# Kernel tuning notes

Hardware: AMD Instinct MI355X
Metric: run time of the kernel (lower is better)

Reference implementation:

```python
import jax, jax.numpy as jnp
import numpy as np

EMBED_DIM = 1024
NUM_HEADS = 16
HEAD_DIM = EMBED_DIM // NUM_HEADS


def setup_inputs() -> dict:
    key = jax.random.key(0)
    ks = jax.random.split(key, 5)
    B, S, D = 2, 2048, EMBED_DIM
    scale_w = 1.0 / np.sqrt(D)
    x = jax.random.normal(ks[0], (B, S, D), dtype=jnp.float32)
    Wq = jax.random.normal(ks[1], (D, D), dtype=jnp.float32) * scale_w
    Wk = jax.random.normal(ks[2], (D, D), dtype=jnp.float32) * scale_w
    Wv = jax.random.normal(ks[3], (D, D), dtype=jnp.float32) * scale_w
    Wo = jax.random.normal(ks[4], (D, D), dtype=jnp.float32) * scale_w
    return {"x": x, "Wq": Wq, "Wk": Wk, "Wv": Wv, "Wo": Wo}


def reference(x, Wq, Wk, Wv, Wo):
    B, S, D = x.shape
    H, Dh = NUM_HEADS, HEAD_DIM
    scale = 1.0 / jnp.sqrt(jnp.asarray(Dh, dtype=x.dtype))

    def split_heads(t):
        return t.reshape(B, S, H, Dh).transpose(0, 2, 1, 3)  # [B,H,S,Dh]

    q = split_heads(x @ Wq)
    k = split_heads(x @ Wk)
    v = split_heads(x @ Wv)

    scores = jnp.einsum("bhqd,bhkd->bhqk", q, k) * scale
    causal = jnp.tril(jnp.ones((S, S), dtype=bool))[None, None]
    scores = jnp.where(causal, scores, jnp.asarray(-1e9, dtype=scores.dtype))
    weights = jax.nn.softmax(scores, axis=-1)
    attn = jnp.einsum("bhqk,bhkd->bhqd", weights, v)
    attn = attn.transpose(0, 2, 1, 3).reshape(B, S, D)
    return attn @ Wo
```

## Files before the change

### kernel.cpp

```cpp
#include <hip/hip_runtime.h>
#include <cstdint>

typedef __bf16 bf16;
typedef __bf16 bf16x2 __attribute__((ext_vector_type(2)));
typedef __bf16 bf16x4 __attribute__((ext_vector_type(4)));
typedef __bf16 bf16x8 __attribute__((ext_vector_type(8)));
typedef float f32x4 __attribute__((ext_vector_type(4)));

constexpr int S = 2048, D = 1024, H = 16, HD = 64, B = 2;
constexpr size_t TSZ = (size_t)B * H * S * HD;

__device__ __forceinline__ f32x4 mfma16(bf16x8 a, bf16x8 b, f32x4 c) {
  return __builtin_amdgcn_mfma_f32_16x16x32_bf16(a, b, c, 0, 0, 0);
}

__device__ __forceinline__ void gl_lds16(const bf16* g, bf16* s) {
  __builtin_amdgcn_global_load_lds((__attribute__((address_space(1))) void*)g,
                                   (__attribute__((address_space(3))) void*)s,
                                   16, 0, 0);
}

__global__ __launch_bounds__(256) void prep_all(const float* __restrict__ x,
                                                const float* __restrict__ W0,
                                                const float* __restrict__ W1,
                                                const float* __restrict__ W2,
                                                const float* __restrict__ W3,
                                                bf16* __restrict__ xb,
                                                bf16* __restrict__ Wt) {
  __shared__ __align__(16) bf16 Lt[64][68];
  const int bid = blockIdx.x, t = threadIdx.x;
  if (bid < 2048) {
    const size_t i = (size_t)bid * 256 + t;
    const float4 a = ((const float4*)x)[2 * i];
    const float4 b = ((const float4*)x)[2 * i + 1];
    bf16x8 o = {(bf16)a.x, (bf16)a.y, (bf16)a.z, (bf16)a.w,
                (bf16)b.x, (bf16)b.y, (bf16)b.z, (bf16)b.w};
    *(bf16x8*)&xb[i * 8] = o;
    return;
  }
  const int r = bid - 2048;
  const int z = r >> 8, rest = r & 255;
  const float* W = z == 0 ? W0 : z == 1 ? W1 : z == 2 ? W2 : W3;
  const int k0 = (rest & 15) * 64, n0 = (rest >> 4) * 64;
  const int tr = t >> 4, tc = (t & 15) * 4;
#pragma unroll
  for (int p = 0; p < 4; ++p) {
    const int rr = 16 * p + tr;
    const float4 v = *(const float4*)&W[(size_t)(k0 + rr) * D + n0 + tc];
    Lt[tc + 0][rr] = (bf16)v.x;
    Lt[tc + 1][rr] = (bf16)v.y;
    Lt[tc + 2][rr] = (bf16)v.z;
    Lt[tc + 3][rr] = (bf16)v.w;
  }
  __syncthreads();
#pragma unroll
  for (int p = 0; p < 4; ++p) {
    const int n = 16 * p + tr;
    const bf16x4 o = *(const bf16x4*)&Lt[n][tc];
    *(bf16x4*)&Wt[((size_t)z * D + n0 + n) * D + k0 + tc] = o;
  }
}

template <int MODE, int BNT>
__global__ __launch_bounds__(256) void gemm_bt(const bf16* __restrict__ A,
                                               const bf16* __restrict__ Bt,
                                               void* __restrict__ Cp) {
  constexpr int K = 1024;
  constexpr int NI = BNT / 32;
  __shared__ __align__(16) bf16 As[128 * 64];
  __shared__ __align__(16) bf16 Bs[BNT * 64];

  const int bid = blockIdx.x, nwg = gridDim.x;
  const int lg = (bid & 7) * (nwg >> 3) + (bid >> 3);
  const int bm = (lg & 31) * 128;
  const int bn = (lg >> 5) * BNT;

  const int t = threadIdx.x, l = t & 63, w = t >> 6;
  const int c = l & 15, g = l >> 4, cx = c & 7;
  const int lrow = l >> 3;
  const int srcc = ((l & 7) ^ lrow) << 3;
  const int wm = (w >> 1) * 64, wn = (w & 1) * (BNT / 2);

  f32x4 acc[4][NI] = {};

  for (int kt = 0; kt < K / 64; ++kt) {
    const int k0 = kt * 64;
    __syncthreads();
#pragma unroll
    for (int i = 0; i < 4; ++i) {
      const int ci = i * 4 + w;
      const int row = ci * 8 + lrow;
      gl_lds16(A + (size_t)(bm + row) * K + k0 + srcc, As + ci * 512 + l * 8);
    }
#pragma unroll
    for (int i = 0; i < BNT / 32; ++i) {
      const int ci = i * 4 + w;
      const int row = ci * 8 + lrow;
      gl_lds16(Bt + (size_t)(bn + row) * K + k0 + srcc, Bs + ci * 512 + l * 8);
    }
    __syncthreads();

    bf16x8 af[4][2], bfv[NI][2];
#pragma unroll
    for (int mi = 0; mi < 4; ++mi) {
      const int row = wm + mi * 16 + c;
#pragma unroll
      for (int kh = 0; kh < 2; ++kh)
        af[mi][kh] = *(const bf16x8*)&As[row * 64 + (((kh * 4 + g) ^ cx) << 3)];
    }
#pragma unroll
    for (int ni = 0; ni < NI; ++ni) {
      const int row = wn + ni * 16 + c;
#pragma unroll
      for (int kh = 0; kh < 2; ++kh)
        bfv[ni][kh] = *(const bf16x8*)&Bs[row * 64 + (((kh * 4 + g) ^ cx) << 3)];
    }
#pragma unroll
    for (int mi = 0; mi < 4; ++mi)
#pragma unroll
      for (int ni = 0; ni < NI; ++ni) {
        acc[mi][ni] = mfma16(af[mi][0], bfv[ni][0], acc[mi][ni]);
        acc[mi][ni] = mfma16(af[mi][1], bfv[ni][1], acc[mi][ni]);
      }
  }

#pragma unroll
  for (int mi = 0; mi < 4; ++mi)
#pragma unroll
    for (int ni = 0; ni < NI; ++ni)
#pragma unroll
      for (int r = 0; r < 4; ++r) {
        const int m = bm + wm + mi * 16 + 4 * g + r;
        const int n = bn + wn + ni * 16 + c;
        const float v = acc[mi][ni][r];
        if constexpr (MODE == 0) {
          const int which = n >> 10, nn = n & 1023;
          const int h = nn >> 6, d = nn & 63;
          const int bb = m >> 11, s = m & 2047;
          ((bf16*)Cp)[which * TSZ + ((((size_t)bb * H + h) * S + s) << 6) + d] =
              (bf16)v;
        } else {
          ((float*)Cp)[(size_t)m * D + n] = v;
        }
      }
}

__global__ __launch_bounds__(256, 4) void attn11(const bf16* __restrict__ Q,
                                                 const bf16* __restrict__ Kg,
                                                 const bf16* __restrict__ Vg,
                                                 bf16* __restrict__ O) {
  __shared__ __align__(16) bf16 Ks[64 * 64];
  __shared__ __align__(16) bf16 Vt[64 * 64];

  const int bid = blockIdx.x;
  const int bh = bid & 31, j = bid >> 5;
  const int t = threadIdx.x, l = t & 63, w = t >> 6;
  const int c = l & 15, g = l >> 4, cx = c & 7;
  const int bb = bh >> 4, h = bh & 15;
  const float SC = 0.18033688011112042f;
  const float THRS = 44.3614195558365f;

  const bf16* Kbase = Kg + (size_t)bh * S * HD;
  const bf16* Vbase = Vg + (size_t)bh * S * HD;

  const int kv0 = t >> 3, dg0 = t & 7;
  const int kv1 = kv0 + 32;
  const int p2 = t & 31, dgv = t >> 5;
  const int hv = p2 >> 4;
  const int gv = (p2 >> 1) & 3;
  const int jv = ((p2 >> 3) & 1) * 4 + (p2 & 1) * 2;
  const int vchunk = (hv << 2) | gv;

  for (int ph = 0; ph < 2; ++ph) {
    const int qt = ph ? (31 - j) : j;
    const int q0 = qt * 64;
    const int qglob = q0 + 16 * w + c;
    const bf16* Qrow = Q + ((size_t)bh * S + qglob) * HD;
    const bf16x8 qf0 = *(const bf16x8*)&Qrow[g * 8];
    const bf16x8 qf1 = *(const bf16x8*)&Qrow[32 + g * 8];

    bf16x8 ka0 = *(const bf16x8*)&Kbase[kv0 * 64 + dg0 * 8];
    bf16x8 ka1 = *(const bf16x8*)&Kbase[kv1 * 64 + dg0 * 8];
    bf16x8 va0 = *(const bf16x8*)&Vbase[(2 * p2) * 64 + dgv * 8];
    bf16x8 va1 = *(const bf16x8*)&Vbase[(2 * p2 + 1) * 64 + dgv * 8];

    f32x4 oacc[4] = {};
    float mrun = -1e30f, lrun = 0.f;

    for (int kt = 0; kt <= qt; ++kt) {
      __builtin_amdgcn_s_barrier();
      __builtin_amdgcn_sched_barrier(0);

      *(bf16x8*)&Ks[kv0 * 64 + ((dg0 ^ (kv0 & 7)) << 3)] = ka0;
      *(bf16x8*)&Ks[kv1 * 64 + ((dg0 ^ (kv1 & 7)) << 3)] = ka1;
#pragma unroll
      for (int i = 0; i < 8; ++i) {
        bf16x2 pr2 = {va0[i], va1[i]};
        *(bf16x2*)&Vt[(8 * dgv + i) * 64 + ((vchunk ^ i) << 3) + jv] = pr2;
      }
      bf16x8 kn0 = ka0, kn1 = ka1, vn0 = va0, vn1 = va1;
      if (kt < qt) {
        const bf16* Kt = Kbase + (size_t)(kt + 1) * 64 * HD;
        const bf16* Vs = Vbase + (size_t)(kt + 1) * 64 * HD;
        kn0 = *(const bf16x8*)&Kt[kv0 * 64 + dg0 * 8];
        kn1 = *(const bf16x8*)&Kt[kv1 * 64 + dg0 * 8];
        vn0 = *(const bf16x8*)&Vs[(2 * p2) * 64 + dgv * 8];
        vn1 = *(const bf16x8*)&Vs[(2 * p2 + 1) * 64 + dgv * 8];
      }
      asm volatile("s_waitcnt lgkmcnt(0)" ::: "memory");
      __builtin_amdgcn_s_barrier();
      __builtin_amdgcn_sched_barrier(0);

      f32x4 st[4];
      __builtin_amdgcn_s_setprio(1);
#pragma unroll
      for (int ct = 0; ct < 4; ++ct) {
        const int krow = ct * 16 + c;
        const bf16x8 kf0 = *(const bf16x8*)&Ks[krow * 64 + ((g ^ cx) << 3)];
        const bf16x8 kf1 = *(const bf16x8*)&Ks[krow * 64 + (((4 + g) ^ cx) << 3)];
        f32x4 z = {};
        z = mfma16(kf0, qf0, z);
        st[ct] = mfma16(kf1, qf1, z);
      }
      __builtin_amdgcn_s_setprio(0);

      if (kt == qt) {
#pragma unroll
        for (int ct = 0; ct < 4; ++ct)
#pragma unroll
          for (int r = 0; r < 4; ++r)
            if (kt * 64 + ct * 16 + 4 * g + r > qglob) st[ct][r] = -1e30f;
      }

      float tm[4];
#pragma unroll
      for (int ct = 0; ct < 4; ++ct)
        tm[ct] = fmaxf(fmaxf(st[ct][0], st[ct][1]), fmaxf(st[ct][2], st[ct][3]));
      float mt = fmaxf(fmaxf(tm[0], tm[1]), fmaxf(tm[2], tm[3]));
      mt = fmaxf(mt, __shfl_xor(mt, 16));
      mt = fmaxf(mt, __shfl_xor(mt, 32));
      if (!__all(mt <= mrun + THRS)) {
        const float mnew = fmaxf(mrun, mt);
        const float fac = __builtin_amdgcn_exp2f((mrun - mnew) * SC);
        lrun *= fac;
#pragma unroll
        for (int ct = 0; ct < 4; ++ct)
#pragma unroll
          for (int r = 0; r < 4; ++r) oacc[ct][r] *= fac;
        mrun = mnew;
      }
      float p[4][4];
      float sq[4];
#pragma unroll
      for (int ct = 0; ct < 4; ++ct) {
#pragma unroll
        for (int r = 0; r < 4; ++r)
          p[ct][r] = __builtin_amdgcn_exp2f((st[ct][r] - mrun) * SC);
        sq[ct] = (p[ct][0] + p[ct][1]) + (p[ct][2] + p[ct][3]);
      }
      lrun += (sq[0] + sq[1]) + (sq[2] + sq[3]);

      const bf16x8 pa0 = {(bf16)p[0][0], (bf16)p[0][1], (bf16)p[0][2], (bf16)p[0][3],
                          (bf16)p[1][0], (bf16)p[1][1], (bf16)p[1][2], (bf16)p[1][3]};
      const bf16x8 pa1 = {(bf16)p[2][0], (bf16)p[2][1], (bf16)p[2][2], (bf16)p[2][3],
                          (bf16)p[3][0], (bf16)p[3][1], (bf16)p[3][2], (bf16)p[3][3]};

      __builtin_amdgcn_s_setprio(1);
#pragma unroll
      for (int ct = 0; ct < 4; ++ct) {
        const int vrow = ct * 16 + c;
        const bf16x8 vt0 = *(const bf16x8*)&Vt[vrow * 64 + ((g ^ cx) << 3)];
        const bf16x8 vt1 = *(const bf16x8*)&Vt[vrow * 64 + (((4 + g) ^ cx) << 3)];
        oacc[ct] = mfma16(vt0, pa0, oacc[ct]);
        oacc[ct] = mfma16(vt1, pa1, oacc[ct]);
      }
      __builtin_amdgcn_s_setprio(0);

      ka0 = kn0; ka1 = kn1; va0 = vn0; va1 = vn1;
    }

    float lt = lrun;
    lt += __shfl_xor(lt, 16);
    lt += __shfl_xor(lt, 32);
    const float inv = 1.f / lt;
    bf16* Orow = O + ((size_t)bb * S + qglob) * D + h * 64;
#pragma unroll
    for (int ct = 0; ct < 4; ++ct)
#pragma unroll
      for (int pr = 0; pr < 2; ++pr) {
        bf16x2 pk = {(bf16)(oacc[ct][2 * pr] * inv),
                     (bf16)(oacc[ct][2 * pr + 1] * inv)};
        *(bf16x2*)&Orow[ct * 16 + 4 * g + 2 * pr] = pk;
      }
  }
}

extern "C" void kernel_launch(void* const* d_in, const int* in_sizes, int n_in,
                              void* d_out, int out_size, void* d_ws, size_t ws_size,
                              hipStream_t stream) {
  const float* x  = (const float*)d_in[0];
  const float* Wq = (const float*)d_in[1];
  const float* Wk = (const float*)d_in[2];
  const float* Wv = (const float*)d_in[3];
  const float* Wo = (const float*)d_in[4];
  float* out = (float*)d_out;

  bf16* xb  = (bf16*)d_ws;
  bf16* Wt  = xb + (size_t)B * S * D;
  bf16* QKV = Wt + (size_t)4 * D * D;
  bf16* Ab  = QKV + 3 * TSZ;

  prep_all<<<3072, 256, 0, stream>>>(x, Wq, Wk, Wv, Wo, xb, Wt);
  gemm_bt<0, 128><<<768, 256, 0, stream>>>(xb, Wt, QKV);
  attn11<<<512, 256, 0, stream>>>(QKV, QKV + TSZ, QKV + 2 * TSZ, Ab);
  gemm_bt<1, 64><<<512, 256, 0, stream>>>(Ab, Wt + (size_t)3 * D * D, out);
}
```

Measured before the change: 98.56 us.

## Split attention KV loop across two wave groups with LDS merge of partial softmax

```diff
diff --git a/kernel.cpp b/kernel.cpp
--- a/kernel.cpp
+++ b/kernel.cpp
@@ -145,16 +145,17 @@
       }
 }
 
-__global__ __launch_bounds__(256, 4) void attn11(const bf16* __restrict__ Q,
+__global__ __launch_bounds__(512, 4) void attn13(const bf16* __restrict__ Q,
                                                  const bf16* __restrict__ Kg,
                                                  const bf16* __restrict__ Vg,
                                                  bf16* __restrict__ O) {
-  __shared__ __align__(16) bf16 Ks[64 * 64];
-  __shared__ __align__(16) bf16 Vt[64 * 64];
+  __shared__ __align__(16) bf16 Ks[2 * 64 * 64];
+  __shared__ __align__(16) bf16 Vt[2 * 64 * 64];
 
   const int bid = blockIdx.x;
   const int bh = bid & 31, j = bid >> 5;
   const int t = threadIdx.x, l = t & 63, w = t >> 6;
+  const int kw = w & 1, qw = w >> 1;
   const int c = l & 15, g = l >> 4, cx = c & 7;
   const int bb = bh >> 4, h = bh & 15;
   const float SC = 0.18033688011112042f;
@@ -164,48 +165,53 @@
   const bf16* Vbase = Vg + (size_t)bh * S * HD;
 
   const int kv0 = t >> 3, dg0 = t & 7;
-  const int kv1 = kv0 + 32;
-  const int p2 = t & 31, dgv = t >> 5;
+  const int th = t >> 8, tt = t & 255;
+  const int p2 = tt & 31, dgv = tt >> 5;
   const int hv = p2 >> 4;
   const int gv = (p2 >> 1) & 3;
   const int jv = ((p2 >> 3) & 1) * 4 + (p2 & 1) * 2;
   const int vchunk = (hv << 2) | gv;
 
+  bf16* KsW = Ks + kw * 4096;
+  bf16* VtW = Vt + kw * 4096;
+  bf16* VtT = Vt + th * 4096;
+
   for (int ph = 0; ph < 2; ++ph) {
     const int qt = ph ? (31 - j) : j;
+    const int nT2 = (qt + 2) >> 1;
     const int q0 = qt * 64;
-    const int qglob = q0 + 16 * w + c;
+    const int qglob = q0 + 16 * qw + c;
     const bf16* Qrow = Q + ((size_t)bh * S + qglob) * HD;
     const bf16x8 qf0 = *(const bf16x8*)&Qrow[g * 8];
     const bf16x8 qf1 = *(const bf16x8*)&Qrow[32 + g * 8];
 
     bf16x8 ka0 = *(const bf16x8*)&Kbase[kv0 * 64 + dg0 * 8];
-    bf16x8 ka1 = *(const bf16x8*)&Kbase[kv1 * 64 + dg0 * 8];
-    bf16x8 va0 = *(const bf16x8*)&Vbase[(2 * p2) * 64 + dgv * 8];
-    bf16x8 va1 = *(const bf16x8*)&Vbase[(2 * p2 + 1) * 64 + dgv * 8];
+    bf16x8 ka1 = *(const bf16x8*)&Kbase[(kv0 + 64) * 64 + dg0 * 8];
+    bf16x8 va0 = *(const bf16x8*)&Vbase[(th * 64 + 2 * p2) * 64 + dgv * 8];
+    bf16x8 va1 = *(const bf16x8*)&Vbase[(th * 64 + 2 * p2 + 1) * 64 + dgv * 8];
 
     f32x4 oacc[4] = {};
     float mrun = -1e30f, lrun = 0.f;
 
-    for (int kt = 0; kt <= qt; ++kt) {
+    for (int kt2 = 0; kt2 < nT2; ++kt2) {
       __builtin_amdgcn_s_barrier();
       __builtin_amdgcn_sched_barrier(0);
 
       *(bf16x8*)&Ks[kv0 * 64 + ((dg0 ^ (kv0 & 7)) << 3)] = ka0;
-      *(bf16x8*)&Ks[kv1 * 64 + ((dg0 ^ (kv1 & 7)) << 3)] = ka1;
+      *(bf16x8*)&Ks[4096 + kv0 * 64 + ((dg0 ^ (kv0 & 7)) << 3)] = ka1;
 #pragma unroll
       for (int i = 0; i < 8; ++i) {
         bf16x2 pr2 = {va0[i], va1[i]};
-        *(bf16x2*)&Vt[(8 * dgv + i) * 64 + ((vchunk ^ i) << 3) + jv] = pr2;
+        *(bf16x2*)&VtT[(8 * dgv + i) * 64 + ((vchunk ^ i) << 3) + jv] = pr2;
       }
       bf16x8 kn0 = ka0, kn1 = ka1, vn0 = va0, vn1 = va1;
-      if (kt < qt) {
-        const bf16* Kt = Kbase + (size_t)(kt + 1) * 64 * HD;
-        const bf16* Vs = Vbase + (size_t)(kt + 1) * 64 * HD;
+      if (kt2 + 1 < nT2) {
+        const bf16* Kt = Kbase + (size_t)(kt2 + 1) * 128 * HD;
+        const bf16* Vs = Vbase + (size_t)(kt2 + 1) * 128 * HD;
         kn0 = *(const bf16x8*)&Kt[kv0 * 64 + dg0 * 8];
-        kn1 = *(const bf16x8*)&Kt[kv1 * 64 + dg0 * 8];
-        vn0 = *(const bf16x8*)&Vs[(2 * p2) * 64 + dgv * 8];
-        vn1 = *(const bf16x8*)&Vs[(2 * p2 + 1) * 64 + dgv * 8];
+        kn1 = *(const bf16x8*)&Kt[(kv0 + 64) * 64 + dg0 * 8];
+        vn0 = *(const bf16x8*)&Vs[(th * 64 + 2 * p2) * 64 + dgv * 8];
+        vn1 = *(const bf16x8*)&Vs[(th * 64 + 2 * p2 + 1) * 64 + dgv * 8];
       }
       asm volatile("s_waitcnt lgkmcnt(0)" ::: "memory");
       __builtin_amdgcn_s_barrier();
@@ -216,20 +222,21 @@
 #pragma unroll
       for (int ct = 0; ct < 4; ++ct) {
         const int krow = ct * 16 + c;
-        const bf16x8 kf0 = *(const bf16x8*)&Ks[krow * 64 + ((g ^ cx) << 3)];
-        const bf16x8 kf1 = *(const bf16x8*)&Ks[krow * 64 + (((4 + g) ^ cx) << 3)];
+        const bf16x8 kf0 = *(const bf16x8*)&KsW[krow * 64 + ((g ^ cx) << 3)];
+        const bf16x8 kf1 = *(const bf16x8*)&KsW[krow * 64 + (((4 + g) ^ cx) << 3)];
         f32x4 z = {};
         z = mfma16(kf0, qf0, z);
         st[ct] = mfma16(kf1, qf1, z);
       }
       __builtin_amdgcn_s_setprio(0);
 
-      if (kt == qt) {
+      if (kt2 == nT2 - 1) {
 #pragma unroll
         for (int ct = 0; ct < 4; ++ct)
 #pragma unroll
           for (int r = 0; r < 4; ++r)
-            if (kt * 64 + ct * 16 + 4 * g + r > qglob) st[ct][r] = -1e30f;
+            if (kt2 * 128 + kw * 64 + ct * 16 + 4 * g + r > qglob)
+              st[ct][r] = -3e38f;
       }
 
       float tm[4];
@@ -269,8 +276,8 @@
 #pragma unroll
       for (int ct = 0; ct < 4; ++ct) {
         const int vrow = ct * 16 + c;
-        const bf16x8 vt0 = *(const bf16x8*)&Vt[vrow * 64 + ((g ^ cx) << 3)];
-        const bf16x8 vt1 = *(const bf16x8*)&Vt[vrow * 64 + (((4 + g) ^ cx) << 3)];
+        const bf16x8 vt0 = *(const bf16x8*)&VtW[vrow * 64 + ((g ^ cx) << 3)];
+        const bf16x8 vt1 = *(const bf16x8*)&VtW[vrow * 64 + (((4 + g) ^ cx) << 3)];
         oacc[ct] = mfma16(vt0, pa0, oacc[ct]);
         oacc[ct] = mfma16(vt1, pa1, oacc[ct]);
       }
@@ -282,16 +289,38 @@
     float lt = lrun;
     lt += __shfl_xor(lt, 16);
     lt += __shfl_xor(lt, 32);
-    const float inv = 1.f / lt;
-    bf16* Orow = O + ((size_t)bb * S + qglob) * D + h * 64;
-#pragma unroll
-    for (int ct = 0; ct < 4; ++ct)
-#pragma unroll
-      for (int pr = 0; pr < 2; ++pr) {
-        bf16x2 pk = {(bf16)(oacc[ct][2 * pr] * inv),
-                     (bf16)(oacc[ct][2 * pr + 1] * inv)};
-        *(bf16x2*)&Orow[ct * 16 + 4 * g + 2 * pr] = pk;
-      }
+
+    float* Ov = (float*)Ks;
+    float* Mv = (float*)Vt;
+    __builtin_amdgcn_s_barrier();
+    __builtin_amdgcn_sched_barrier(0);
+    if (kw == 1) {
+#pragma unroll
+      for (int ct = 0; ct < 4; ++ct)
+        *(f32x4*)&Ov[qw * 1024 + l * 16 + (((ct + l) & 3) << 2)] = oacc[ct];
+      if (g == 0) { Mv[qw * 32 + 2 * c] = mrun; Mv[qw * 32 + 2 * c + 1] = lt; }
+    }
+    asm volatile("s_waitcnt lgkmcnt(0)" ::: "memory");
+    __builtin_amdgcn_s_barrier();
+    __builtin_amdgcn_sched_barrier(0);
+    if (kw == 0) {
+      const float m2 = Mv[qw * 32 + 2 * c], l2 = Mv[qw * 32 + 2 * c + 1];
+      const float mn = fmaxf(mrun, m2);
+      const float f0 = __builtin_amdgcn_exp2f((mrun - mn) * SC);
+      const float f1 = __builtin_amdgcn_exp2f((m2 - mn) * SC);
+      const float inv = 1.f / (lt * f0 + l2 * f1);
+      bf16* Orow = O + ((size_t)bb * S + qglob) * D + h * 64;
+#pragma unroll
+      for (int ct = 0; ct < 4; ++ct) {
+        const f32x4 o2 = *(const f32x4*)&Ov[qw * 1024 + l * 16 + (((ct + l) & 3) << 2)];
+#pragma unroll
+        for (int pr = 0; pr < 2; ++pr) {
+          bf16x2 pk = {(bf16)((oacc[ct][2 * pr] * f0 + o2[2 * pr] * f1) * inv),
+                       (bf16)((oacc[ct][2 * pr + 1] * f0 + o2[2 * pr + 1] * f1) * inv)};
+          *(bf16x2*)&Orow[ct * 16 + 4 * g + 2 * pr] = pk;
+        }
+      }
+    }
   }
 }
 
@@ -312,6 +341,6 @@
 
   prep_all<<<3072, 256, 0, stream>>>(x, Wq, Wk, Wv, Wo, xb, Wt);
   gemm_bt<0, 128><<<768, 256, 0, stream>>>(xb, Wt, QKV);
-  attn11<<<512, 256, 0, stream>>>(QKV, QKV + TSZ, QKV + 2 * TSZ, Ab);
+  attn13<<<512, 512, 0, stream>>>(QKV, QKV + TSZ, QKV + 2 * TSZ, Ab);
   gemm_bt<1, 64><<<512, 256, 0, stream>>>(Ab, Wt + (size_t)3 * D * D, out);
 }
```

After: 101.6 us. +3.1%, slower.
